# Optimization experiments

Hardware: AMD Instinct MI355X
Metric: run time of the kernel (lower is better)

Reference implementation:

```python
import jax, jax.numpy as jnp
import numpy as np

N, L, H, D = 2, 4096, 12, 64
HD = H * D

def setup_inputs() -> dict:
    key = jax.random.key(0)
    ks = jax.random.split(key, 5)
    s = 1.0 / np.sqrt(HD)  # keep projections well-scaled
    return {
        "x": jax.random.normal(ks[0], (N, L, HD), dtype=jnp.float32),
        "Wq": jax.random.normal(ks[1], (HD, HD), dtype=jnp.float32) * s,
        "bq": jnp.zeros((HD,), dtype=jnp.float32),
        "Wk": jax.random.normal(ks[2], (HD, HD), dtype=jnp.float32) * s,
        "bk": jnp.zeros((HD,), dtype=jnp.float32),
        "Wv": jax.random.normal(ks[3], (HD, HD), dtype=jnp.float32) * s,
        "bv": jnp.zeros((HD,), dtype=jnp.float32),
        "Wo": jax.random.normal(ks[4], (HD, HD), dtype=jnp.float32) * s,
        "bo": jnp.zeros((HD,), dtype=jnp.float32),
        "train": 0,
    }

def reference(x, Wq, bq, Wk, bk, Wv, bv, Wo, bo, train):
    n, l, hd = x.shape
    h, d = H, D
    # QKV projections (hk.Linear: x @ W + b), reshape to (n, l, h, d)
    q = (x @ Wq + bq).reshape(n, l, h, d)
    k = (x @ Wk + bk).reshape(n, l, h, d)
    v = (x @ Wv + bv).reshape(n, l, h, d)
    # scores: (n, q, k, h), scaled by sqrt(key_size)
    qkt = jnp.einsum('nqhd,nkhd->nqkh', q, k) / jnp.sqrt(jnp.float32(d))
    attn = jax.nn.softmax(qkt, axis=2)
    # eval mode: dropout_rate is 0.0, so dropout is identity
    o = jnp.einsum('nqkh,nkhd->nqhd', attn, v).reshape(n, l, hd)
    return o @ Wo + bo
```

## Files before the change

### kernel.cpp

```cpp
#include <hip/hip_runtime.h>

#define NN 2
#define LL 4096
#define HH 12
#define DD 64
#define HD_ 768
#define M_TOT (NN * LL)
#define KVSTRIDE 262144

typedef __bf16 bf16_t;
typedef _Float16 f16_t;
typedef __bf16 bf16x8 __attribute__((ext_vector_type(8)));
typedef __bf16 bf16x4 __attribute__((ext_vector_type(4)));
typedef _Float16 f16x2 __attribute__((ext_vector_type(2)));
typedef _Float16 f16x4 __attribute__((ext_vector_type(4)));
typedef _Float16 f16x8 __attribute__((ext_vector_type(8)));
typedef float floatx4 __attribute__((ext_vector_type(4)));
typedef float floatx16 __attribute__((ext_vector_type(16)));

#define QSCALE 0.1803368801111f

__device__ __forceinline__ void async_load16(const void* g, void* l) {
    __builtin_amdgcn_global_load_lds(
        (const __attribute__((address_space(1))) unsigned int*)(g),
        (__attribute__((address_space(3))) unsigned int*)(l),
        16, 0, 0);
}

__device__ __forceinline__ f16x2 pkrtz(float a, float b) {
    return __builtin_bit_cast(f16x2, __builtin_amdgcn_cvt_pkrtz(a, b));
}

__global__ void cvt_kernel(const float* __restrict__ src, bf16_t* __restrict__ dst, int n4) {
    int i = blockIdx.x * blockDim.x + threadIdx.x;
    if (i < n4) {
        const float4 v = ((const float4*)src)[i];
        bf16_t* d = dst + (size_t)i * 4;
        d[0] = (bf16_t)v.x; d[1] = (bf16_t)v.y; d[2] = (bf16_t)v.z; d[3] = (bf16_t)v.w;
    }
}

struct WtArgs { const float* W[4]; bf16_t* Wt[4]; };
__global__ __launch_bounds__(256) void cvt_wt_kernel(WtArgs a) {
    __shared__ bf16_t T[64 * 65];
    const int z = blockIdx.z;
    const int k0 = blockIdx.y * 64, n0 = blockIdx.x * 64;
    const int tid = threadIdx.x;
    {
        const int k = tid >> 2;
        const int nc = (tid & 3) * 16;
        const float* src = a.W[z] + (size_t)(k0 + k) * HD_ + n0 + nc;
        for (int i = 0; i < 4; ++i) {
            float4 v = *(const float4*)(src + i * 4);
            T[(nc + i * 4 + 0) * 65 + k] = (bf16_t)v.x;
            T[(nc + i * 4 + 1) * 65 + k] = (bf16_t)v.y;
            T[(nc + i * 4 + 2) * 65 + k] = (bf16_t)v.z;
            T[(nc + i * 4 + 3) * 65 + k] = (bf16_t)v.w;
        }
    }
    __syncthreads();
    {
        const int n = tid >> 2;
        const int kc = (tid & 3) * 16;
        bf16_t* dst = a.Wt[z] + (size_t)(n0 + n) * HD_ + k0 + kc;
        bf16x8 v0, v1;
        for (int j = 0; j < 8; ++j) { v0[j] = T[n * 65 + kc + j]; v1[j] = T[n * 65 + kc + 8 + j]; }
        *(bf16x8*)dst = v0;
        *(bf16x8*)(dst + 8) = v1;
    }
}

__device__ __forceinline__ void gemm_tile128(
    const bf16_t* __restrict__ A, const bf16_t* __restrict__ Bt,
    bf16_t* As, bf16_t* Bs, int m0, int n0, floatx4 (&acc)[4][4])
{
    const int tid  = threadIdx.x;
    const int w    = tid >> 6, lane = tid & 63;
    const int quad = lane >> 4, l16 = lane & 15;
    const int wm = w >> 1, wn = w & 1;
    const int rsub = lane >> 3;
    const int csub = (lane & 7) * 8;

    const bf16_t* aBase = A + (size_t)(m0 + w * 32 + rsub) * HD_ + csub;
    const bf16_t* bBase = Bt + (size_t)(n0 + w * 32 + rsub) * HD_ + csub;

    for (int kt = 0; kt < HD_; kt += 64) {
        __syncthreads();
        for (int i = 0; i < 4; ++i) {
            const int ar = w * 32 + i * 8;
            async_load16(aBase + (size_t)i * 8 * HD_ + kt, As + ar * 64 + lane * 8);
            async_load16(bBase + (size_t)i * 8 * HD_ + kt, Bs + ar * 64 + lane * 8);
        }
        __syncthreads();
        for (int ks = 0; ks < 2; ++ks) {
            bf16x8 af[4], bf[4];
            for (int mi = 0; mi < 4; ++mi)
                af[mi] = *(const bf16x8*)&As[(wm * 64 + mi * 16 + l16) * 64 + ks * 32 + quad * 8];
            for (int ni = 0; ni < 4; ++ni)
                bf[ni] = *(const bf16x8*)&Bs[(wn * 64 + ni * 16 + l16) * 64 + ks * 32 + quad * 8];
            for (int mi = 0; mi < 4; ++mi)
                for (int ni = 0; ni < 4; ++ni)
                    acc[mi][ni] = __builtin_amdgcn_mfma_f32_16x16x32_bf16(
                        af[mi], bf[ni], acc[mi][ni], 0, 0, 0);
        }
    }
}

struct QKVArgs {
    const bf16_t* Bt[3];
    const float* bias[3];
    void* out[3];
};
__global__ __launch_bounds__(256) void gemm_qkv_kernel(const bf16_t* __restrict__ A, QKVArgs p)
{
    __shared__ __align__(16) bf16_t S[2 * 128 * 64];
    const int z = blockIdx.z;
    const int m0 = blockIdx.y * 128, n0 = blockIdx.x * 128;

    floatx4 acc[4][4] = {};
    gemm_tile128(A, p.Bt[z], S, S + 8192, m0, n0, acc);

    const int tid  = threadIdx.x;
    const int lane = tid & 63;
    const int quad = lane >> 4, l16 = lane & 15;
    const int w    = tid >> 6;
    const int wm = w >> 1, wn = w & 1;
    const float scale = (z == 0) ? QSCALE : 1.0f;
    const float* bias = p.bias[z];

    __syncthreads();
    for (int ni = 0; ni < 4; ++ni) {
        const int dl = ni * 16 + l16;
        const float bv = bias[n0 + wn * 64 + dl];
        for (int mi = 0; mi < 4; ++mi) {
            for (int r = 0; r < 4; ++r) {
                const int ll = wm * 64 + mi * 16 + quad * 4 + r;
                const float val = (acc[mi][ni][r] + bv) * scale;
                int off;
                if (z == 0)
                    off = ll * 64 + dl;
                else if (z == 1)
                    off = ((ll >> 5) * 4 + (dl >> 4)) * 512
                        + ((ll & 31) + 32 * ((dl >> 3) & 1)) * 8 + (dl & 7);
                else
                    off = (((ll >> 6) * 2 + (dl >> 5)) * 4 + ((ll >> 4) & 3)) * 512
                        + ((dl & 31) + 32 * ((ll >> 2) & 1)) * 8
                        + ((ll & 3) + 4 * ((ll >> 3) & 1));
                if (z == 2) ((f16_t*)S)[wn * 8192 + off] = (f16_t)val;
                else        S[wn * 8192 + off] = (bf16_t)val;
            }
        }
    }
    __syncthreads();

    const int ht = tid >> 7, idx = tid & 127;
    const int nn = m0 >> 12, l0 = m0 & 4095;
    const int h = (n0 >> 6) + ht;
    char* dstBase;
    if (z == 0)
        dstBase = (char*)p.out[0] + (((size_t)(nn * HH + h) * LL + l0) * 64) * 2;
    else if (z == 1)
        dstBase = (char*)p.out[1] + ((size_t)(nn * HH + h) * KVSTRIDE + (size_t)(l0 >> 5) * 2048) * 2;
    else
        dstBase = (char*)p.out[2] + ((size_t)(nn * HH + h) * KVSTRIDE + (size_t)(l0 >> 6) * 4096) * 2;
    const bf16_t* srcB = S + ht * 8192;
    for (int c = 0; c < 8; ++c) {
        const int cc = (c + idx) & 7;
        *(bf16x8*)(dstBase + (idx * 64 + cc * 8) * 2) = *(const bf16x8*)(srcB + idx * 64 + cc * 8);
    }
}

__global__ __launch_bounds__(256) void gemm_o_kernel(
    const bf16_t* __restrict__ A, const bf16_t* __restrict__ Bt,
    const float* __restrict__ bias, float* __restrict__ Cout)
{
    __shared__ __align__(16) bf16_t As[128 * 64];
    __shared__ __align__(16) bf16_t Bs[64 * 64];
    const int m0 = blockIdx.y * 128, n0 = blockIdx.x * 64;

    const int tid  = threadIdx.x;
    const int w    = tid >> 6, lane = tid & 63;
    const int quad = lane >> 4, l16 = lane & 15;
    const int rsub = lane >> 3;
    const int csub = (lane & 7) * 8;

    const bf16_t* aBase = A + (size_t)(m0 + w * 32 + rsub) * HD_ + csub;
    const bf16_t* bBase = Bt + (size_t)(n0 + w * 16 + rsub) * HD_ + csub;

    floatx4 acc[2][4] = {};

    for (int kt = 0; kt < HD_; kt += 64) {
        __syncthreads();
        #pragma unroll
        for (int i = 0; i < 4; ++i)
            async_load16(aBase + (size_t)i * 8 * HD_ + kt, As + (w * 32 + i * 8) * 64 + lane * 8);
        #pragma unroll
        for (int i = 0; i < 2; ++i)
            async_load16(bBase + (size_t)i * 8 * HD_ + kt, Bs + (w * 16 + i * 8) * 64 + lane * 8);
        __syncthreads();
        #pragma unroll
        for (int ks = 0; ks < 2; ++ks) {
            bf16x8 af[2], bf[4];
            #pragma unroll
            for (int mi = 0; mi < 2; ++mi)
                af[mi] = *(const bf16x8*)&As[(w * 32 + mi * 16 + l16) * 64 + ks * 32 + quad * 8];
            #pragma unroll
            for (int ni = 0; ni < 4; ++ni)
                bf[ni] = *(const bf16x8*)&Bs[(ni * 16 + l16) * 64 + ks * 32 + quad * 8];
            #pragma unroll
            for (int mi = 0; mi < 2; ++mi)
                #pragma unroll
                for (int ni = 0; ni < 4; ++ni)
                    acc[mi][ni] = __builtin_amdgcn_mfma_f32_16x16x32_bf16(
                        af[mi], bf[ni], acc[mi][ni], 0, 0, 0);
        }
    }

    #pragma unroll
    for (int ni = 0; ni < 4; ++ni) {
        const int col = n0 + ni * 16 + l16;
        const float bv = bias[col];
        #pragma unroll
        for (int mi = 0; mi < 2; ++mi)
            #pragma unroll
            for (int r = 0; r < 4; ++r) {
                const int row = m0 + w * 32 + mi * 16 + quad * 4 + r;
                Cout[(size_t)row * HD_ + col] = acc[mi][ni][r] + bv;
            }
    }
}

__global__ __launch_bounds__(256, 3) void attn_kernel(
    const bf16_t* __restrict__ qg, const bf16_t* __restrict__ kf,
    const f16_t* __restrict__ vf, bf16_t* __restrict__ og)
{
    __shared__ union {
        struct {
            bf16_t Ks[2][4096];
            f16_t  Vs[4][4096];
        } s;
        bf16_t OT[128 * 72];
    } u;

    const int tid = threadIdx.x;
    const int w = tid >> 6, lane = tid & 63;
    const int l32 = lane & 31, hi = lane >> 5;

    const int lb = blockIdx.y * gridDim.x + blockIdx.x;
    const int idx = (lb & 7) * 96 + (lb >> 3);
    const int nh = idx >> 5;
    const int qt0 = (idx & 31) * 128;
    const int nIdx = nh / HH, hIdx = nh % HH;

    bf16x8 qfrag[4];
    {
        const bf16_t* qp = qg + ((size_t)nh * LL + qt0 + w * 32 + l32) * DD + hi * 8;
        for (int s = 0; s < 4; ++s) qfrag[s] = *(const bf16x8*)(qp + s * 16);
    }

    const bf16_t* ksrc = kf + (size_t)nh * KVSTRIDE + (2 * w) * 512 + lane * 8;
    const f16_t*  vsrc = vf + (size_t)nh * KVSTRIDE + (2 * w) * 512 + lane * 8;
    const int soff0 = (2 * w) * 512 + lane * 8;
    const int soff1 = (2 * w + 1) * 512 + lane * 8;

    floatx16 oacc[2] = {};
    float rs = 0.f;
    floatx16 sA0, sA1, sB0, sB1;

#define STAGE_K(kb) { async_load16(ksrc, &u.s.Ks[kb][soff0]);                 \
                      async_load16(ksrc + 512, &u.s.Ks[kb][soff1]);           \
                      ksrc += 4096; }
#define STAGE_V(vb) { async_load16(vsrc, &u.s.Vs[vb][soff0]);                 \
                      async_load16(vsrc + 512, &u.s.Vs[vb][soff1]);           \
                      vsrc += 4096; }

#define SSTEP(SD0, SD1, kr)                                                   \
    {                                                                         \
        SD0 = (floatx16){}; SD1 = (floatx16){};                               \
        _Pragma("unroll")                                                     \
        for (int s = 0; s < 4; ++s) {                                         \
            bf16x8 a0 = *(const bf16x8*)&u.s.Ks[kr][s * 512 + lane * 8];      \
            SD0 = __builtin_amdgcn_mfma_f32_32x32x16_bf16(a0, qfrag[s], SD0, 0, 0, 0); \
            bf16x8 a1 = *(const bf16x8*)&u.s.Ks[kr][(4 + s) * 512 + lane * 8]; \
            SD1 = __builtin_amdgcn_mfma_f32_32x32x16_bf16(a1, qfrag[s], SD1, 0, 0, 0); \
        }                                                                     \
    }

#define PHALF(SC, vp, kvb)                                                    \
    _Pragma("unroll")                                                         \
    for (int sub = 0; sub < 2; ++sub) {                                       \
        float p[8];                                                           \
        _Pragma("unroll")                                                     \
        for (int i = 0; i < 8; ++i)                                           \
            p[i] = __builtin_amdgcn_exp2f(SC[(kvb) * 0 + sub * 8 + i]);       \
        rs += ((p[0] + p[1]) + (p[2] + p[3])) + ((p[4] + p[5]) + (p[6] + p[7])); \
        f16x2 ab = pkrtz(p[0], p[1]), cd = pkrtz(p[2], p[3]);                 \
        f16x2 ef = pkrtz(p[4], p[5]), gh = pkrtz(p[6], p[7]);                 \
        f16x4 lo4 = __builtin_shufflevector(ab, cd, 0, 1, 2, 3);              \
        f16x4 hi4 = __builtin_shufflevector(ef, gh, 0, 1, 2, 3);              \
        f16x8 pf = __builtin_shufflevector(lo4, hi4, 0, 1, 2, 3, 4, 5, 6, 7); \
        const int kstep = (kvb) * 2 + sub;                                    \
        _Pragma("unroll")                                                     \
        for (int db = 0; db < 2; ++db) {                                      \
            f16x8 av = *(const f16x8*)&u.s.Vs[vp][(db * 4 + kstep) * 512 + lane * 8]; \
            oacc[db] = __builtin_amdgcn_mfma_f32_32x32x16_f16(av, pf, oacc[db], 0, 0, 0); \
        }                                                                     \
    }

#define STEP(doDMA, kw, vw, doS, kr, SD0, SD1, SP0, SP1, vp)                  \
    __syncthreads();                                                          \
    if (doDMA) { STAGE_K(kw); STAGE_V(vw); }                                  \
    __builtin_amdgcn_s_setprio(1);                                            \
    if (doS) SSTEP(SD0, SD1, kr);                                             \
    PHALF(SP0, vp, 0)                                                         \
    PHALF(SP1, vp, 1)                                                         \
    __builtin_amdgcn_s_setprio(0);

    STAGE_K(0) STAGE_V(0) STAGE_K(1) STAGE_V(1)
    __syncthreads();
    SSTEP(sA0, sA1, 0);

    for (int t = 0; t < 60; t += 4) {
        STEP(1, 0, 2, 1, 1, sB0, sB1, sA0, sA1, 0)
        STEP(1, 1, 3, 1, 0, sA0, sA1, sB0, sB1, 1)
        STEP(1, 0, 0, 1, 1, sB0, sB1, sA0, sA1, 2)
        STEP(1, 1, 1, 1, 0, sA0, sA1, sB0, sB1, 3)
    }
    STEP(1, 0, 2, 1, 1, sB0, sB1, sA0, sA1, 0)
    STEP(1, 1, 3, 1, 0, sA0, sA1, sB0, sB1, 1)
    STEP(0, 0, 0, 1, 1, sB0, sB1, sA0, sA1, 2)
    STEP(0, 0, 0, 0, 0, sA0, sA1, sB0, sB1, 3)

#undef STEP
#undef PHALF
#undef SSTEP
#undef STAGE_K
#undef STAGE_V

    rs += __shfl_xor(rs, 32);
    const float rinv = __builtin_amdgcn_rcpf(rs);

    __syncthreads();
    for (int db = 0; db < 2; ++db)
        for (int g = 0; g < 4; ++g) {
            bf16x4 o4;
            for (int r = 0; r < 4; ++r)
                o4[r] = (bf16_t)(oacc[db][g * 4 + r] * rinv);
            *(bf16x4*)&u.OT[(w * 32 + l32) * 72 + db * 32 + hi * 4 + g * 8] = o4;
        }
    __syncthreads();

    const int q = tid >> 1, hf = tid & 1;
    const bf16_t* src = &u.OT[q * 72 + hf * 32];
    bf16x8 r0 = *(const bf16x8*)(src + 0);
    bf16x8 r1 = *(const bf16x8*)(src + 8);
    bf16x8 r2 = *(const bf16x8*)(src + 16);
    bf16x8 r3 = *(const bf16x8*)(src + 24);
    bf16_t* dst = og + ((size_t)nIdx * LL + qt0 + q) * HD_ + hIdx * 64 + hf * 32;
    *(bf16x8*)(dst + 0)  = r0;
    *(bf16x8*)(dst + 8)  = r1;
    *(bf16x8*)(dst + 16) = r2;
    *(bf16x8*)(dst + 24) = r3;
}

extern "C" void kernel_launch(void* const* d_in, const int* in_sizes, int n_in,
                              void* d_out, int out_size, void* d_ws, size_t ws_size,
                              hipStream_t stream) {
    const float* x  = (const float*)d_in[0];
    const float* Wq = (const float*)d_in[1];
    const float* bq = (const float*)d_in[2];
    const float* Wk = (const float*)d_in[3];
    const float* bk = (const float*)d_in[4];
    const float* Wv = (const float*)d_in[5];
    const float* bv = (const float*)d_in[6];
    const float* Wo = (const float*)d_in[7];
    const float* bo = (const float*)d_in[8];

    char* ws = (char*)d_ws;
    const size_t xbytes = (size_t)M_TOT * HD_ * 2;
    const size_t wbytes = (size_t)HD_ * HD_ * 2;

    bf16_t* xb  = (bf16_t*)ws; ws += xbytes;
    bf16_t* wqt = (bf16_t*)ws; ws += wbytes;
    bf16_t* wkt = (bf16_t*)ws; ws += wbytes;
    bf16_t* wvt = (bf16_t*)ws; ws += wbytes;
    bf16_t* wot = (bf16_t*)ws; ws += wbytes;
    bf16_t* qb  = (bf16_t*)ws; ws += xbytes;
    bf16_t* kfb = (bf16_t*)ws; ws += xbytes;
    f16_t*  vfb = (f16_t*)ws;  ws += xbytes;
    bf16_t* ob  = (bf16_t*)ws; ws += xbytes;

    cvt_kernel<<<(M_TOT * HD_ / 4 + 255) / 256, 256, 0, stream>>>(x, xb, M_TOT * HD_ / 4);

    WtArgs wa;
    wa.W[0] = Wq; wa.W[1] = Wk; wa.W[2] = Wv; wa.W[3] = Wo;
    wa.Wt[0] = wqt; wa.Wt[1] = wkt; wa.Wt[2] = wvt; wa.Wt[3] = wot;
    cvt_wt_kernel<<<dim3(12, 12, 4), 256, 0, stream>>>(wa);

    QKVArgs qa;
    qa.Bt[0] = wqt; qa.Bt[1] = wkt; qa.Bt[2] = wvt;
    qa.bias[0] = bq; qa.bias[1] = bk; qa.bias[2] = bv;
    qa.out[0] = qb; qa.out[1] = kfb; qa.out[2] = vfb;
    gemm_qkv_kernel<<<dim3(HD_ / 128, M_TOT / 128, 3), 256, 0, stream>>>(xb, qa);

    attn_kernel<<<dim3(LL / 128, NN * HH), 256, 0, stream>>>(qb, kfb, vfb, ob);

    gemm_o_kernel<<<dim3(HD_ / 64, M_TOT / 128), 256, 0, stream>>>(ob, wot, bo, (float*)d_out);
}
```

Measured before the change: 297.9 us.

## Load V fragments directly to registers and merge conversion prep kernels

The attention kernel stops staging V tiles through shared memory. Each step now loads the next tile's V fragments straight from global memory into registers, double-buffered across even and odd steps, while K keeps its async LDS double buffer. This cuts LDS use to the two K buffers (raising possible occupancy) and drops LDS reads for V, at the cost of more VGPRs and exposed global-load latency. Separately, the x conversion and the weight transpose/convert kernels are merged into a single launch to save one kernel launch.

```diff
diff --git a/kernel.cpp b/kernel.cpp
--- a/kernel.cpp
+++ b/kernel.cpp
@@ -31,21 +31,22 @@
     return __builtin_bit_cast(f16x2, __builtin_amdgcn_cvt_pkrtz(a, b));
 }
 
-__global__ void cvt_kernel(const float* __restrict__ src, bf16_t* __restrict__ dst, int n4) {
-    int i = blockIdx.x * blockDim.x + threadIdx.x;
-    if (i < n4) {
-        const float4 v = ((const float4*)src)[i];
-        bf16_t* d = dst + (size_t)i * 4;
+struct PrepArgs { const float* x; bf16_t* xb; const float* W[4]; bf16_t* Wt[4]; };
+#define CVT_BLOCKS 6144
+__global__ __launch_bounds__(256) void prep_kernel(PrepArgs a) {
+    __shared__ bf16_t T[64 * 65];
+    const int bid = blockIdx.x;
+    const int tid = threadIdx.x;
+    if (bid < CVT_BLOCKS) {
+        const int i = bid * 256 + tid;
+        const float4 v = ((const float4*)a.x)[i];
+        bf16_t* d = a.xb + (size_t)i * 4;
         d[0] = (bf16_t)v.x; d[1] = (bf16_t)v.y; d[2] = (bf16_t)v.z; d[3] = (bf16_t)v.w;
-    }
-}
-
-struct WtArgs { const float* W[4]; bf16_t* Wt[4]; };
-__global__ __launch_bounds__(256) void cvt_wt_kernel(WtArgs a) {
-    __shared__ bf16_t T[64 * 65];
-    const int z = blockIdx.z;
-    const int k0 = blockIdx.y * 64, n0 = blockIdx.x * 64;
-    const int tid = threadIdx.x;
+        return;
+    }
+    int r = bid - CVT_BLOCKS;
+    const int z = r / 144; r -= z * 144;
+    const int k0 = (r / 12) * 64, n0 = (r % 12) * 64;
     {
         const int k = tid >> 2;
         const int nc = (tid & 3) * 16;
@@ -235,10 +236,7 @@
     const f16_t* __restrict__ vf, bf16_t* __restrict__ og)
 {
     __shared__ union {
-        struct {
-            bf16_t Ks[2][4096];
-            f16_t  Vs[4][4096];
-        } s;
+        bf16_t Ks[2][4096];
         bf16_t OT[128 * 72];
     } u;
 
@@ -259,40 +257,42 @@
     }
 
     const bf16_t* ksrc = kf + (size_t)nh * KVSTRIDE + (2 * w) * 512 + lane * 8;
-    const f16_t*  vsrc = vf + (size_t)nh * KVSTRIDE + (2 * w) * 512 + lane * 8;
     const int soff0 = (2 * w) * 512 + lane * 8;
     const int soff1 = (2 * w + 1) * 512 + lane * 8;
+
+    const f16_t* vbase = vf + (size_t)nh * KVSTRIDE + lane * 8;
 
     floatx16 oacc[2] = {};
     float rs = 0.f;
     floatx16 sA0, sA1, sB0, sB1;
-
-#define STAGE_K(kb) { async_load16(ksrc, &u.s.Ks[kb][soff0]);                 \
-                      async_load16(ksrc + 512, &u.s.Ks[kb][soff1]);           \
+    f16x8 va[8], vb[8];
+
+#define STAGE_K(kb) { async_load16(ksrc, &u.Ks[kb][soff0]);                   \
+                      async_load16(ksrc + 512, &u.Ks[kb][soff1]);             \
                       ksrc += 4096; }
-#define STAGE_V(vb) { async_load16(vsrc, &u.s.Vs[vb][soff0]);                 \
-                      async_load16(vsrc + 512, &u.s.Vs[vb][soff1]);           \
-                      vsrc += 4096; }
+#define VLOAD(VR, T) { const f16_t* vp = vbase + (size_t)(T) * 4096;          \
+        _Pragma("unroll")                                                     \
+        for (int i = 0; i < 8; ++i) VR[i] = *(const f16x8*)(vp + i * 512); }
 
 #define SSTEP(SD0, SD1, kr)                                                   \
     {                                                                         \
         SD0 = (floatx16){}; SD1 = (floatx16){};                               \
         _Pragma("unroll")                                                     \
         for (int s = 0; s < 4; ++s) {                                         \
-            bf16x8 a0 = *(const bf16x8*)&u.s.Ks[kr][s * 512 + lane * 8];      \
+            bf16x8 a0 = *(const bf16x8*)&u.Ks[kr][s * 512 + lane * 8];        \
             SD0 = __builtin_amdgcn_mfma_f32_32x32x16_bf16(a0, qfrag[s], SD0, 0, 0, 0); \
-            bf16x8 a1 = *(const bf16x8*)&u.s.Ks[kr][(4 + s) * 512 + lane * 8]; \
+            bf16x8 a1 = *(const bf16x8*)&u.Ks[kr][(4 + s) * 512 + lane * 8];  \
             SD1 = __builtin_amdgcn_mfma_f32_32x32x16_bf16(a1, qfrag[s], SD1, 0, 0, 0); \
         }                                                                     \
     }
 
-#define PHALF(SC, vp, kvb)                                                    \
+#define PHALF(SC, VR, kvb)                                                    \
     _Pragma("unroll")                                                         \
     for (int sub = 0; sub < 2; ++sub) {                                       \
         float p[8];                                                           \
         _Pragma("unroll")                                                     \
         for (int i = 0; i < 8; ++i)                                           \
-            p[i] = __builtin_amdgcn_exp2f(SC[(kvb) * 0 + sub * 8 + i]);       \
+            p[i] = __builtin_amdgcn_exp2f(SC[sub * 8 + i]);                   \
         rs += ((p[0] + p[1]) + (p[2] + p[3])) + ((p[4] + p[5]) + (p[6] + p[7])); \
         f16x2 ab = pkrtz(p[0], p[1]), cd = pkrtz(p[2], p[3]);                 \
         f16x2 ef = pkrtz(p[4], p[5]), gh = pkrtz(p[6], p[7]);                 \
@@ -301,41 +301,49 @@
         f16x8 pf = __builtin_shufflevector(lo4, hi4, 0, 1, 2, 3, 4, 5, 6, 7); \
         const int kstep = (kvb) * 2 + sub;                                    \
         _Pragma("unroll")                                                     \
-        for (int db = 0; db < 2; ++db) {                                      \
-            f16x8 av = *(const f16x8*)&u.s.Vs[vp][(db * 4 + kstep) * 512 + lane * 8]; \
-            oacc[db] = __builtin_amdgcn_mfma_f32_32x32x16_f16(av, pf, oacc[db], 0, 0, 0); \
-        }                                                                     \
-    }
-
-#define STEP(doDMA, kw, vw, doS, kr, SD0, SD1, SP0, SP1, vp)                  \
+        for (int db = 0; db < 2; ++db)                                        \
+            oacc[db] = __builtin_amdgcn_mfma_f32_32x32x16_f16(                \
+                VR[db * 4 + kstep], pf, oacc[db], 0, 0, 0);                   \
+    }
+
+#define STEP_E(T, doV, doK, doS)                                              \
     __syncthreads();                                                          \
-    if (doDMA) { STAGE_K(kw); STAGE_V(vw); }                                  \
+    if (doV) VLOAD(vb, (T) + 1);                                              \
+    if (doK) STAGE_K(0);                                                      \
     __builtin_amdgcn_s_setprio(1);                                            \
-    if (doS) SSTEP(SD0, SD1, kr);                                             \
-    PHALF(SP0, vp, 0)                                                         \
-    PHALF(SP1, vp, 1)                                                         \
+    if (doS) SSTEP(sB0, sB1, 1);                                              \
+    PHALF(sA0, va, 0) PHALF(sA1, va, 1)                                       \
     __builtin_amdgcn_s_setprio(0);
 
-    STAGE_K(0) STAGE_V(0) STAGE_K(1) STAGE_V(1)
+#define STEP_O(T, doV, doK, doS)                                              \
+    __syncthreads();                                                          \
+    if (doV) VLOAD(va, (T) + 1);                                              \
+    if (doK) STAGE_K(1);                                                      \
+    __builtin_amdgcn_s_setprio(1);                                            \
+    if (doS) SSTEP(sA0, sA1, 0);                                              \
+    PHALF(sB0, vb, 0) PHALF(sB1, vb, 1)                                       \
+    __builtin_amdgcn_s_setprio(0);
+
+    STAGE_K(0) STAGE_K(1)
+    VLOAD(va, 0);
     __syncthreads();
     SSTEP(sA0, sA1, 0);
 
-    for (int t = 0; t < 60; t += 4) {
-        STEP(1, 0, 2, 1, 1, sB0, sB1, sA0, sA1, 0)
-        STEP(1, 1, 3, 1, 0, sA0, sA1, sB0, sB1, 1)
-        STEP(1, 0, 0, 1, 1, sB0, sB1, sA0, sA1, 2)
-        STEP(1, 1, 1, 1, 0, sA0, sA1, sB0, sB1, 3)
-    }
-    STEP(1, 0, 2, 1, 1, sB0, sB1, sA0, sA1, 0)
-    STEP(1, 1, 3, 1, 0, sA0, sA1, sB0, sB1, 1)
-    STEP(0, 0, 0, 1, 1, sB0, sB1, sA0, sA1, 2)
-    STEP(0, 0, 0, 0, 0, sA0, sA1, sB0, sB1, 3)
-
-#undef STEP
+    for (int t = 0; t < 60; t += 2) {
+        STEP_E(t, 1, 1, 1)
+        STEP_O(t + 1, 1, 1, 1)
+    }
+    STEP_E(60, 1, 1, 1)
+    STEP_O(61, 1, 1, 1)
+    STEP_E(62, 1, 0, 1)
+    STEP_O(63, 0, 0, 0)
+
+#undef STEP_E
+#undef STEP_O
 #undef PHALF
 #undef SSTEP
+#undef VLOAD
 #undef STAGE_K
-#undef STAGE_V
 
     rs += __shfl_xor(rs, 32);
     const float rinv = __builtin_amdgcn_rcpf(rs);
@@ -390,12 +398,11 @@
     f16_t*  vfb = (f16_t*)ws;  ws += xbytes;
     bf16_t* ob  = (bf16_t*)ws; ws += xbytes;
 
-    cvt_kernel<<<(M_TOT * HD_ / 4 + 255) / 256, 256, 0, stream>>>(x, xb, M_TOT * HD_ / 4);
-
-    WtArgs wa;
-    wa.W[0] = Wq; wa.W[1] = Wk; wa.W[2] = Wv; wa.W[3] = Wo;
-    wa.Wt[0] = wqt; wa.Wt[1] = wkt; wa.Wt[2] = wvt; wa.Wt[3] = wot;
-    cvt_wt_kernel<<<dim3(12, 12, 4), 256, 0, stream>>>(wa);
+    PrepArgs pa;
+    pa.x = x; pa.xb = xb;
+    pa.W[0] = Wq; pa.W[1] = Wk; pa.W[2] = Wv; pa.W[3] = Wo;
+    pa.Wt[0] = wqt; pa.Wt[1] = wkt; pa.Wt[2] = wvt; pa.Wt[3] = wot;
+    prep_kernel<<<CVT_BLOCKS + 576, 256, 0, stream>>>(pa);
 
     QKVArgs qa;
     qa.Bt[0] = wqt; qa.Bt[1] = wkt; qa.Bt[2] = wvt;
```

Result: slower. 387.1 us (+29.9%).
